# Performance work log

Measured on AMD Instinct MI355X. Metric: run time of the kernel, lower is better.

The kernel has to match this reference:

```python
import jax, jax.numpy as jnp
import numpy as np

B, L = 8, 512
D_MODEL, N_HEADS, N_LAYERS = 768, 12, 12
D_HEAD = D_MODEL // N_HEADS
D_FF = 4 * D_MODEL
NUM_LABELS = 1000
PATCH_DIM = 16 * 16 * 3
EPS = 1e-6


def setup_inputs() -> dict:
    key = jax.random.key(0)
    ks = jax.random.split(key, 24)
    d = D_MODEL

    def w(k, shape, fan_in):
        return (jax.random.normal(k, shape, jnp.float32) / np.sqrt(fan_in)).astype(jnp.float32)

    return {
        'patch': jax.random.normal(ks[0], (B, L, PATCH_DIM), jnp.float32),
        'box': jax.random.uniform(ks[1], (B, L, 4), jnp.float32),
        'patch_W': w(ks[2], (PATCH_DIM, d), PATCH_DIM),
        'patch_b': jnp.zeros((d,), jnp.float32),
        'box_W': w(ks[3], (d, d), d),
        'box_b': jnp.zeros((d,), jnp.float32),
        'Wq': w(ks[4], (N_LAYERS, d, d), d),
        'Wk': w(ks[5], (N_LAYERS, d, d), d),
        'Wv': w(ks[6], (N_LAYERS, d, d), d),
        'Wo': w(ks[7], (N_LAYERS, d, d), d),
        'attn_norm_w': jnp.ones((N_LAYERS, d), jnp.float32),
        'gate_W': w(ks[8], (N_LAYERS, d, D_FF), d),
        'hidden_W': w(ks[9], (N_LAYERS, d, D_FF), d),
        'ffn_out_W': w(ks[10], (N_LAYERS, D_FF, d), D_FF),
        'ffn_norm_w': jnp.ones((N_LAYERS, d), jnp.float32),
        'reward_norm_w': jnp.ones((d,), jnp.float32),
        'reward_W': w(ks[11], (d, 2), d),
        'reward_b': jnp.zeros((2,), jnp.float32),
        'label_norm_w': jnp.ones((d,), jnp.float32),
        'label_W': w(ks[12], (d, NUM_LABELS), d),
        'label_b': jnp.zeros((NUM_LABELS,), jnp.float32),
        'box_norm_w': jnp.ones((d,), jnp.float32),
        'boxh_W': w(ks[13], (d, 4), d),
        'boxh_b': jnp.zeros((4,), jnp.float32),
    }


def _rmsnorm(x, wgt):
    return x * jax.lax.rsqrt(jnp.mean(x * x, axis=-1, keepdims=True) + EPS) * wgt


def _rope(x, cos, sin):
    # x: [b, n, l, dh]; consecutive pairs form complex numbers (view_as_complex)
    xr, xi = x[..., 0::2], x[..., 1::2]
    out_r = xr * cos - xi * sin
    out_i = xr * sin + xi * cos
    return jnp.stack((out_r, out_i), axis=-1).reshape(x.shape)


def _forward(patch, box, patch_W, patch_b, box_W, box_b, Wq, Wk, Wv, Wo,
             attn_norm_w, gate_W, hidden_W, ffn_out_W, ffn_norm_w,
             reward_norm_w, reward_W, reward_b, label_norm_w, label_W, label_b,
             box_norm_w, boxh_W, boxh_b):
    b, l, _ = patch.shape
    d = D_MODEL
    # StackedSinusoidalEmbedding(d_model, 4): d_stack = d/4, theta over d_stack/2 freqs
    d_stack = d // 4
    theta_box = 1.0 / (10000.0 ** (2.0 * jnp.arange(d_stack // 2, dtype=jnp.float32) / d_stack))
    ang = box[..., None] * theta_box  # [b, l, 4, d_stack/2]
    box_sin = jnp.stack((jnp.cos(ang), jnp.sin(ang)), axis=-1).reshape(b, l, d)

    x = (patch @ patch_W + patch_b) + (box_sin @ box_W + box_b)

    # RoPE tables and causal mask (constants)
    theta = 1.0 / (10000.0 ** (2.0 * jnp.arange(D_HEAD // 2, dtype=jnp.float32) / D_HEAD))
    pos_ang = jnp.arange(l, dtype=jnp.float32)[:, None] * theta  # [l, dh/2]
    cos, sin = jnp.cos(pos_ang), jnp.sin(pos_ang)
    mask = jnp.triu(jnp.full((l, l), -jnp.inf, dtype=jnp.float32), 1)
    scale = jnp.float32(np.sqrt(D_HEAD))

    def block(h, p):
        wq, wk, wv, wo, anw, gw, hw, ow, fnw = p
        hn = _rmsnorm(h, anw)
        q = (hn @ wq).reshape(b, l, N_HEADS, D_HEAD).transpose(0, 2, 1, 3)
        k = (hn @ wk).reshape(b, l, N_HEADS, D_HEAD).transpose(0, 2, 1, 3)
        v = (hn @ wv).reshape(b, l, N_HEADS, D_HEAD).transpose(0, 2, 1, 3)
        scores = jnp.einsum('bnld,bnmd->bnlm', _rope(q, cos, sin), _rope(k, cos, sin)) / scale
        attn = jax.nn.softmax(scores + mask, axis=-1)
        o = jnp.einsum('bnlm,bnmd->bnld', attn, v).transpose(0, 2, 1, 3).reshape(b, l, d)
        h = h + o @ wo
        hn = _rmsnorm(h, fnw)
        h = h + (jax.nn.silu(hn @ gw) * (hn @ hw)) @ ow
        return h, None

    x, _ = jax.lax.scan(block, x, (Wq, Wk, Wv, Wo, attn_norm_w, gate_W, hidden_W, ffn_out_W, ffn_norm_w))

    reward = _rmsnorm(x, reward_norm_w) @ reward_W + reward_b
    label = _rmsnorm(x, label_norm_w) @ label_W + label_b
    box_out = _rmsnorm(x, box_norm_w) @ boxh_W + boxh_b
    return reward, label, box_out


def reference(patch, box, patch_W, patch_b, box_W, box_b, Wq, Wk, Wv, Wo,
              attn_norm_w, gate_W, hidden_W, ffn_out_W, ffn_norm_w,
              reward_norm_w, reward_W, reward_b, label_norm_w, label_W, label_b,
              box_norm_w, boxh_W, boxh_b):
    return _forward(patch, box, patch_W, patch_b, box_W, box_b, Wq, Wk, Wv, Wo,
                    attn_norm_w, gate_W, hidden_W, ffn_out_W, ffn_norm_w,
                    reward_norm_w, reward_W, reward_b, label_norm_w, label_W, label_b,
                    box_norm_w, boxh_W, boxh_b)
```

## Files before the change

### kernel.cpp

```cpp
#include <hip/hip_runtime.h>
#include <math.h>
#include <type_traits>

#define B_   8
#define L_   512
#define MTOK 4096
#define D_   768
#define NH_  12
#define DH_  64
#define DFF_ 3072
#define NL_  12

typedef unsigned short u16;
typedef __attribute__((ext_vector_type(4))) float f32x4;
typedef __attribute__((ext_vector_type(8))) short i16x8;
typedef __attribute__((ext_vector_type(8))) __bf16 b16x8;

template <typename A, typename = void>
struct PickFrag { using type = i16x8; };
template <typename A>
struct PickFrag<A, std::void_t<decltype(__builtin_amdgcn_mfma_f32_16x16x32_bf16(
    std::declval<A>(), std::declval<A>(), std::declval<f32x4>(), 0, 0, 0))>> {
  using type = A;
};
using frag_t = typename PickFrag<b16x8>::type;

#if __has_builtin(__builtin_amdgcn_global_load_lds)
#define HAS_GLDS 1
#else
#define HAS_GLDS 0
#endif

__device__ inline u16 f2bf(float f) {
    unsigned u = __float_as_uint(f);
    unsigned r = u + 0x7fffu + ((u >> 16) & 1u);
    return (u16)(r >> 16);
}
__device__ inline float bf2f(u16 b) { return __uint_as_float(((unsigned)b) << 16); }

__device__ inline void bar_raw() {
    asm volatile("" ::: "memory");
    __builtin_amdgcn_s_barrier();
    asm volatile("" ::: "memory");
}

__device__ inline int swz8(int row, int c8) { return c8 ^ ((row & 7) << 3); }

__device__ inline void glds16(const u16* g, u16* l) {
#if HAS_GLDS
    __builtin_amdgcn_global_load_lds(
        (const __attribute__((address_space(1))) void*)g,
        (__attribute__((address_space(3))) void*)l, 16, 0, 0);
#else
    *reinterpret_cast<uint4*>(l) = *reinterpret_cast<const uint4*>(g);
#endif
}

__global__ void k_box_sin(u16* __restrict__ emb, const float* __restrict__ box) {
    int idx = blockIdx.x * blockDim.x + threadIdx.x;
    if (idx >= MTOK * D_) return;
    int t = idx / D_, d = idx % D_;
    int c = d / 192, r = d % 192, j = r >> 1;
    float theta = __expf(-(float)j * (9.210340371976184f / 96.0f));
    float ang = box[t * 4 + c] * theta;
    emb[(size_t)t * 1536 + 768 + d] = f2bf((r & 1) ? sinf(ang) : cosf(ang));
}

__global__ void k_cast(u16* __restrict__ emb, const float* __restrict__ in, int n4) {
    int i = blockIdx.x * blockDim.x + threadIdx.x;
    if (i >= n4) return;
    int t = i / 192, c4 = (i % 192) * 4;
    float4 v = *reinterpret_cast<const float4*>(in + (size_t)t * 768 + c4);
    unsigned lo = (unsigned)f2bf(v.x) | ((unsigned)f2bf(v.y) << 16);
    unsigned hi = (unsigned)f2bf(v.z) | ((unsigned)f2bf(v.w) << 16);
    *reinterpret_cast<uint2*>(emb + (size_t)t * 1536 + c4) = make_uint2(lo, hi);
}

__global__ void k_addb(float* __restrict__ dst, const float* __restrict__ a,
                       const float* __restrict__ b) {
    int i = blockIdx.x * blockDim.x + threadIdx.x;
    if (i < D_) dst[i] = a[i] + b[i];
}

__global__ __launch_bounds__(256) void k_convT(u16* __restrict__ dst,
                                               const float* __restrict__ src,
                                               int K, int N, int ld, int rs,
                                               int ro, int co) {
    __shared__ float t[32][33];
    int bn = blockIdx.x * 32;
    int bk = blockIdx.y * 32;
    int tx = threadIdx.x % 32, ty = threadIdx.x / 32;
    #pragma unroll
    for (int i = 0; i < 4; ++i) {
        int k = bk + ty + i * 8;
        int n = bn + tx;
        t[ty + i * 8][tx] = (n < N) ? src[(size_t)k * N + n] : 0.0f;
    }
    __syncthreads();
    #pragma unroll
    for (int i = 0; i < 4; ++i) {
        int n = bn + ty + i * 8;
        int k = bk + tx;
        dst[(size_t)(n * rs + ro) * ld + co + k] = f2bf(t[tx][ty + i * 8]);
    }
}


__global__ __launch_bounds__(256) void k_convT128(u16* __restrict__ dst,
                                                  const float* __restrict__ src,
                                                  int K, int N) {
    __shared__ float ts[32][131];
    const float* s = src + (size_t)blockIdx.z * K * N;
    u16* d = dst + (size_t)blockIdx.z * K * N;
    int bn = blockIdx.x * 32, bk = blockIdx.y * 128;
    int t = threadIdx.x, rn = t & 31, kr = t >> 5;
    #pragma unroll
    for (int p = 0; p < 16; ++p) {
        int k = p * 8 + kr;
        ts[rn][k] = s[(size_t)(bk + k) * N + bn + rn];
    }
    __syncthreads();
    int n = t >> 3, c = (t & 7) * 8;
    u16 ta[8], tb[8];
    #pragma unroll
    for (int j = 0; j < 8; ++j) ta[j] = f2bf(ts[n][c + j]);
    #pragma unroll
    for (int j = 0; j < 8; ++j) tb[j] = f2bf(ts[n][64 + c + j]);
    u16* dp = &d[(size_t)(bn + n) * K + bk];
    *reinterpret_cast<uint4*>(dp + c)      = *reinterpret_cast<uint4*>(ta);
    *reinterpret_cast<uint4*>(dp + 64 + c) = *reinterpret_cast<uint4*>(tb);
}

__global__ __launch_bounds__(256) void k_convT128_qkv(u16* __restrict__ dst,
                                                      const float* __restrict__ s0,
                                                      const float* __restrict__ s1,
                                                      const float* __restrict__ s2) {
    __shared__ float ts[32][131];
    int ly = blockIdx.z / 3, which = blockIdx.z % 3;
    const float* s = (which == 0 ? s0 : (which == 1 ? s1 : s2)) + (size_t)ly * 768 * 768;
    u16* d = dst + ((size_t)ly * 3 + which) * 768 * 768;
    int bn = blockIdx.x * 32, bk = blockIdx.y * 128;
    int t = threadIdx.x, rn = t & 31, kr = t >> 5;
    #pragma unroll
    for (int p = 0; p < 16; ++p) {
        int k = p * 8 + kr;
        ts[rn][k] = s[(size_t)(bk + k) * 768 + bn + rn];
    }
    __syncthreads();
    int n = t >> 3, c = (t & 7) * 8;
    u16 ta[8], tb[8];
    #pragma unroll
    for (int j = 0; j < 8; ++j) ta[j] = f2bf(ts[n][c + j]);
    #pragma unroll
    for (int j = 0; j < 8; ++j) tb[j] = f2bf(ts[n][64 + c + j]);
    u16* dp = &d[(size_t)(bn + n) * 768 + bk];
    *reinterpret_cast<uint4*>(dp + c)      = *reinterpret_cast<uint4*>(ta);
    *reinterpret_cast<uint4*>(dp + 64 + c) = *reinterpret_cast<uint4*>(tb);
}

__global__ __launch_bounds__(256) void k_convT128_gh(u16* __restrict__ dst,
                                                     const float* __restrict__ g,
                                                     const float* __restrict__ h) {
    __shared__ float ts[32][131];
    int ly = blockIdx.z >> 1, which = blockIdx.z & 1;
    const float* s = (which ? h : g) + (size_t)ly * 768 * 3072;
    u16* d = dst + (size_t)ly * 6144 * 768;
    int bn = blockIdx.x * 32, bk = blockIdx.y * 128;
    int t = threadIdx.x, rn = t & 31, kr = t >> 5;
    #pragma unroll
    for (int p = 0; p < 16; ++p) {
        int k = p * 8 + kr;
        ts[rn][k] = s[(size_t)(bk + k) * 3072 + bn + rn];
    }
    __syncthreads();
    int n = t >> 3, c = (t & 7) * 8;
    int ng = bn + n;
    int row = ((ng >> 4) << 5) + (ng & 15) + which * 16;
    u16 ta[8], tb[8];
    #pragma unroll
    for (int j = 0; j < 8; ++j) ta[j] = f2bf(ts[n][c + j]);
    #pragma unroll
    for (int j = 0; j < 8; ++j) tb[j] = f2bf(ts[n][64 + c + j]);
    u16* dp = &d[(size_t)row * 768 + bk];
    *reinterpret_cast<uint4*>(dp + c)      = *reinterpret_cast<uint4*>(ta);
    *reinterpret_cast<uint4*>(dp + 64 + c) = *reinterpret_cast<uint4*>(tb);
}

template <int S>
__global__ __launch_bounds__(192) void k_fused_rr(float* __restrict__ h,
                                                  const float* __restrict__ part,
                                                  u16* __restrict__ hn,
                                                  const float* __restrict__ w) {
    int t = blockIdx.x;
    int i4 = threadIdx.x;
    size_t b4 = (size_t)t * 192 + i4;
    float4 v = reinterpret_cast<const float4*>(h)[b4];
    #pragma unroll
    for (int s = 0; s < S; ++s) {
        float4 p = reinterpret_cast<const float4*>(part + (size_t)s * MTOK * D_)[b4];
        v.x += p.x; v.y += p.y; v.z += p.z; v.w += p.w;
    }
    if (S > 0) reinterpret_cast<float4*>(h)[b4] = v;
    float ss = v.x * v.x + v.y * v.y + v.z * v.z + v.w * v.w;
    for (int off = 32; off > 0; off >>= 1) ss += __shfl_down(ss, off);
    __shared__ float red[3];
    int wid = threadIdx.x >> 6, lane = threadIdx.x & 63;
    if (lane == 0) red[wid] = ss;
    __syncthreads();
    float inv = rsqrtf((red[0] + red[1] + red[2]) / (float)D_ + 1e-6f);
    float4 wv = reinterpret_cast<const float4*>(w)[i4];
    unsigned lo = (unsigned)f2bf(v.x * inv * wv.x) | ((unsigned)f2bf(v.y * inv * wv.y) << 16);
    unsigned hi = (unsigned)f2bf(v.z * inv * wv.z) | ((unsigned)f2bf(v.w * inv * wv.w) << 16);
    *reinterpret_cast<uint2*>(hn + (size_t)t * D_ + i4 * 4) = make_uint2(lo, hi);
}

__global__ void k_rope_tab(float* __restrict__ tab) {
    int idx = blockIdx.x * blockDim.x + threadIdx.x;
    if (idx >= L_ * 32) return;
    int l = idx >> 5, j = idx & 31;
    float theta = __expf(-(float)j * (9.210340371976184f / 32.0f));
    float s, c;
    sincosf((float)l * theta, &s, &c);
    tab[idx * 2] = c;
    tab[idx * 2 + 1] = s;
}

__global__ __launch_bounds__(512) void k_gemm512_gh(u16* __restrict__ Cp,
                                                    const u16* __restrict__ A,
                                                    const u16* __restrict__ BT,
                                                    int K, int ldC) {
    __shared__ u16 smem[32768];
    int tid = threadIdx.x;
    int wid = tid >> 6, lane = tid & 63;

    int nx = gridDim.x, ny = gridDim.y;
    int bid = blockIdx.y * nx + blockIdx.x;
    int nwg = nx * ny;
    int cpx = nwg >> 3;
    int swzb = (bid & 7) * cpx + (bid >> 3);
    int by = swzb / nx, bx = swzb % nx;
    int row0 = by * 256, col0 = bx * 256;
    int wr = wid >> 2, wcn = wid & 3;

    int c0 = tid, c1 = tid + 512;
    int r0 = c0 >> 2, r1 = c1 >> 2;
    int gsrc = (((tid & 3) ^ ((tid >> 3) & 3)) << 3);
    const u16* gA0 = A  + (size_t)(row0 + r0) * K + gsrc;
    const u16* gA1 = A  + (size_t)(row0 + r1) * K + gsrc;
    const u16* gB0 = BT + (size_t)(col0 + r0) * K + gsrc;
    const u16* gB1 = BT + (size_t)(col0 + r1) * K + gsrc;

    auto stage = [&](int buf, int kt) {
        u16* Asb = smem + buf * 8192;
        u16* Bsb = smem + 16384 + buf * 8192;
        glds16(gA0 + kt, &Asb[c0 * 8]);
        glds16(gA1 + kt, &Asb[c1 * 8]);
        glds16(gB0 + kt, &Bsb[c0 * 8]);
        glds16(gB1 + kt, &Bsb[c1 * 8]);
    };

    f32x4 acc[8][4] = {};
    int lr = lane & 15, lg = lane >> 4;
    int lk = (((lg ^ ((lr >> 1) & 3))) << 3);

    stage(0, 0);
    int cur = 0;
    for (int kt = 0; kt < K; kt += 32) {
        bool has_next = (kt + 32 < K);
        if (has_next) stage(cur ^ 1, kt + 32);
        if (has_next) asm volatile("s_waitcnt vmcnt(4) lgkmcnt(0)" ::: "memory");
        else          asm volatile("s_waitcnt vmcnt(0) lgkmcnt(0)" ::: "memory");
        __builtin_amdgcn_sched_barrier(0);
        bar_raw();
        const u16* Asb = smem + cur * 8192;
        const u16* Bsb = smem + 16384 + cur * 8192;
        frag_t af[8], bfr[4];
        #pragma unroll
        for (int m = 0; m < 8; ++m)
            af[m] = *reinterpret_cast<const frag_t*>(&Asb[(wr * 128 + m * 16 + lr) * 32 + lk]);
        #pragma unroll
        for (int n = 0; n < 4; ++n)
            bfr[n] = *reinterpret_cast<const frag_t*>(&Bsb[(wcn * 64 + n * 16 + lr) * 32 + lk]);
        #pragma unroll
        for (int m = 0; m < 8; ++m)
            #pragma unroll
            for (int n = 0; n < 4; ++n)
                acc[m][n] = __builtin_amdgcn_mfma_f32_16x16x32_bf16(af[m], bfr[n], acc[m][n], 0, 0, 0);
        bar_raw();
        cur ^= 1;
    }

    int lcol = lane & 15, rb = (lane >> 4) * 4;
    #pragma unroll
    for (int m = 0; m < 8; ++m) {
        #pragma unroll
        for (int np = 0; np < 2; ++np) {
            int ocol = (col0 >> 1) + wcn * 32 + np * 16 + lcol;
            #pragma unroll
            for (int e = 0; e < 4; ++e) {
                int row = row0 + wr * 128 + m * 16 + rb + e;
                float g = acc[m][2 * np][e], hv = acc[m][2 * np + 1][e];
                float s = g / (1.0f + __expf(-g));
                Cp[(size_t)row * ldC + ocol] = f2bf(s * hv);
            }
        }
    }
}

template <int MODE>
__global__ __launch_bounds__(256) void k_gemm_bf16(void* __restrict__ Cp,
                                                   const u16* __restrict__ A,
                                                   const u16* __restrict__ BT,
                                                   const float* __restrict__ bias,
                                                   int K, int Nout, int ldC) {
    __shared__ u16 smem[16384];
    int tid = threadIdx.x;
    int wid = tid >> 6, lane = tid & 63;

    int nx = gridDim.x, ny = gridDim.y, nz = gridDim.z;
    int bid = ((blockIdx.z * ny) + blockIdx.y) * nx + blockIdx.x;
    int nwg = nx * ny * nz;
    int cpx = nwg >> 3;
    int swz = (bid & 7) * cpx + (bid >> 3);
    int sk  = swz / (nx * ny);
    int rem = swz % (nx * ny);
    int by = rem / nx, bx = rem % nx;
    int row0 = by * 128, col0 = bx * 128;
    int wr = wid >> 1, wc = wid & 1;

    int Klen = K / nz;
    int kbeg = sk * Klen;

    int c0 = wid * 128 + lane;
    int c1 = c0 + 64;
    int r0 = c0 >> 2, kc0 = (c0 & 3) * 8;
    int r1 = c1 >> 2, kc1 = (c1 & 3) * 8;
    const u16* gA0 = A  + (size_t)(row0 + r0) * K + kbeg + kc0;
    const u16* gA1 = A  + (size_t)(row0 + r1) * K + kbeg + kc1;
    const u16* gB0 = BT + (size_t)(col0 + r0) * K + kbeg + kc0;
    const u16* gB1 = BT + (size_t)(col0 + r1) * K + kbeg + kc1;

    auto stage = [&](int buf, int kt) {
        u16* Asb = smem + buf * 4096;
        u16* Bsb = smem + 8192 + buf * 4096;
        glds16(gA0 + kt, &Asb[c0 * 8]);
        glds16(gA1 + kt, &Asb[c1 * 8]);
        glds16(gB0 + kt, &Bsb[c0 * 8]);
        glds16(gB1 + kt, &Bsb[c1 * 8]);
    };

    f32x4 acc[4][4] = {};
    int lrow = lane & 15, lk = (lane >> 4) * 8;

    stage(0, 0);
    int cur = 0;
    for (int kt = 0; kt < Klen; kt += 32) {
        bool has_next = (kt + 32 < Klen);
        if (has_next) stage(cur ^ 1, kt + 32);
        if (has_next) asm volatile("s_waitcnt vmcnt(4) lgkmcnt(0)" ::: "memory");
        else          asm volatile("s_waitcnt vmcnt(0) lgkmcnt(0)" ::: "memory");
        __builtin_amdgcn_sched_barrier(0);
        bar_raw();
        const u16* Asb = smem + cur * 4096;
        const u16* Bsb = smem + 8192 + cur * 4096;
        frag_t af[4], bfr[4];
        #pragma unroll
        for (int m = 0; m < 4; ++m)
            af[m] = *reinterpret_cast<const frag_t*>(&Asb[(wr * 64 + m * 16 + lrow) * 32 + lk]);
        #pragma unroll
        for (int n = 0; n < 4; ++n)
            bfr[n] = *reinterpret_cast<const frag_t*>(&Bsb[(wc * 64 + n * 16 + lrow) * 32 + lk]);
        #pragma unroll
        for (int m = 0; m < 4; ++m)
            #pragma unroll
            for (int n = 0; n < 4; ++n)
                acc[m][n] = __builtin_amdgcn_mfma_f32_16x16x32_bf16(af[m], bfr[n], acc[m][n], 0, 0, 0);
        bar_raw();
        cur ^= 1;
    }

    int lcol = lane & 15, rb = (lane >> 4) * 4;

    if (MODE == 6) {
        u16* qkvh = (u16*)Cp;
        const float* tab = bias;
        if (col0 >= 1536) {
            int head_base = (col0 - 1536) >> 6;
            int bb = row0 >> 9;
            int l0 = row0 & 511;
            #pragma unroll
            for (int pass = 0; pass < 2; ++pass) {
                if (wc == pass) {
                    #pragma unroll
                    for (int m = 0; m < 4; ++m) {
                        #pragma unroll
                        for (int n = 0; n < 4; ++n) {
                            int dl = n * 16 + lcol;
                            int rl = wr * 64 + m * 16 + rb;
                            u16 tmp[4];
                            #pragma unroll
                            for (int e = 0; e < 4; ++e) tmp[e] = f2bf(acc[m][n][e]);
                            *reinterpret_cast<uint2*>(&smem[dl * 136 + rl]) =
                                *reinterpret_cast<uint2*>(tmp);
                        }
                    }
                }
                __syncthreads();
                int head = head_base + pass;
                size_t vbase = (size_t)2 * MTOK * 768 +
                               ((size_t)(bb * NH_ + head) * 64) * 512;
                #pragma unroll
                for (int it = 0; it < 4; ++it) {
                    int dd = it * 16 + (tid >> 4);
                    int rr = (tid & 15) * 8;
                    uint4 v4 = *reinterpret_cast<const uint4*>(&smem[dd * 136 + rr]);
                    *reinterpret_cast<uint4*>(&qkvh[vbase + (size_t)dd * 512 + l0 + rr]) = v4;
                }
                __syncthreads();
            }
        } else {
            int sec = col0 / 768;
            float qscale = (sec == 0) ? 0.125f : 1.0f;
            #pragma unroll
            for (int m = 0; m < 4; ++m) {
                #pragma unroll
                for (int n = 0; n < 4; ++n) {
                    int col = col0 + wc * 64 + n * 16 + lcol;
                    int head = (col % 768) >> 6;
                    int d = col & 63;
                    #pragma unroll
                    for (int e = 0; e < 4; ++e) {
                        int row = row0 + wr * 64 + m * 16 + rb + e;
                        int bb = row >> 9, l = row & 511;
                        float v = acc[m][n][e];
                        float p = __shfl_xor(v, 1);
                        float2 cs = *reinterpret_cast<const float2*>(
                            tab + ((size_t)l * 32 + (d >> 1)) * 2);
                        float r = (d & 1) ? (p * cs.y + v * cs.x)
                                          : (v * cs.x - p * cs.y);
                        r *= qscale;
                        qkvh[(size_t)sec * MTOK * 768 +
                             ((size_t)(bb * NH_ + head) * 512 + l) * 64 + d] = f2bf(r);
                    }
                }
            }
        }
        return;
    }

    float* Cpart = (MODE == 4)
        ? ((float*)Cp + (size_t)sk * (size_t)(ny * 128) * ldC) : (float*)Cp;
    #pragma unroll
    for (int m = 0; m < 4; ++m) {
        #pragma unroll
        for (int n = 0; n < 4; ++n) {
            int col = col0 + wc * 64 + n * 16 + lcol;
            if (col >= Nout) continue;
            #pragma unroll
            for (int e = 0; e < 4; ++e) {
                int row = row0 + wr * 64 + m * 16 + rb + e;
                float v = acc[m][n][e];
                size_t off = (size_t)row * ldC + col;
                if (MODE == 0) {
                    if (bias) v += bias[col];
                    ((float*)Cp)[off] = v;
                } else if (MODE == 3) {
                    ((u16*)Cp)[off] = f2bf(v);
                } else if (MODE == 4) {
                    Cpart[off] = v;
                }
            }
        }
    }
}

__global__ __launch_bounds__(256) void k_attn3(u16* __restrict__ o,
                                               const u16* __restrict__ qh,
                                               const u16* __restrict__ kh,
                                               const u16* __restrict__ vT) {
    int bh = blockIdx.x, qb = blockIdx.y;
    int b = bh / NH_, hh = bh % NH_;
    int tid = threadIdx.x, wid = tid >> 6, lane = tid & 63;
    __shared__ u16 Qs[64][72], Ps[64][72];
    __shared__ u16 Ks[64 * 64], Vs[64 * 64];

    #pragma unroll
    for (int i = 0; i < 2; ++i) {
        int idx = tid + i * 256;
        int r = idx >> 3, c8 = (idx & 7) * 8;
        uint4 v4 = *reinterpret_cast<const uint4*>(
            qh + ((size_t)bh * L_ + qb * 64 + r) * 64 + c8);
        *reinterpret_cast<uint4*>(&Qs[r][c8]) = v4;
    }
    __syncthreads();

    int lr = lane & 15, lg = lane >> 4;
    frag_t aq[2];
    #pragma unroll
    for (int kd = 0; kd < 2; ++kd)
        aq[kd] = *reinterpret_cast<const frag_t*>(&Qs[wid * 16 + lr][kd * 32 + lg * 8]);

    int sr0 = tid >> 3, sc8 = (tid & 7) * 8;
    int sr1 = sr0 + 32;

    f32x4 accO[4] = {};
    float M[4], S[4];
    #pragma unroll
    for (int e = 0; e < 4; ++e) { M[e] = -INFINITY; S[e] = 0.f; }

    uint4 kreg0 = *reinterpret_cast<const uint4*>(kh + ((size_t)bh * L_ + sr0) * 64 + sc8);
    uint4 kreg1 = *reinterpret_cast<const uint4*>(kh + ((size_t)bh * L_ + sr1) * 64 + sc8);
    uint4 vreg0 = *reinterpret_cast<const uint4*>(vT + ((size_t)bh * 64 + sr0) * L_ + sc8);
    uint4 vreg1 = *reinterpret_cast<const uint4*>(vT + ((size_t)bh * 64 + sr1) * L_ + sc8);

    for (int kb = 0; kb <= qb; ++kb) {
        __syncthreads();
        *reinterpret_cast<uint4*>(&Ks[sr0 * 64 + swz8(sr0, sc8)]) = kreg0;
        *reinterpret_cast<uint4*>(&Ks[sr1 * 64 + swz8(sr1, sc8)]) = kreg1;
        *reinterpret_cast<uint4*>(&Vs[sr0 * 64 + swz8(sr0, sc8)]) = vreg0;
        *reinterpret_cast<uint4*>(&Vs[sr1 * 64 + swz8(sr1, sc8)]) = vreg1;
        __syncthreads();
        if (kb < qb) {
            int nb = (kb + 1) * 64;
            kreg0 = *reinterpret_cast<const uint4*>(kh + ((size_t)bh * L_ + nb + sr0) * 64 + sc8);
            kreg1 = *reinterpret_cast<const uint4*>(kh + ((size_t)bh * L_ + nb + sr1) * 64 + sc8);
            vreg0 = *reinterpret_cast<const uint4*>(vT + ((size_t)bh * 64 + sr0) * L_ + nb + sc8);
            vreg1 = *reinterpret_cast<const uint4*>(vT + ((size_t)bh * 64 + sr1) * L_ + nb + sc8);
        }

        f32x4 sv[4];
        __builtin_amdgcn_s_setprio(1);
        #pragma unroll
        for (int ct = 0; ct < 4; ++ct) {
            int krow = ct * 16 + lr;
            frag_t bk0 = *reinterpret_cast<const frag_t*>(&Ks[krow * 64 + swz8(krow, lg * 8)]);
            frag_t bk1 = *reinterpret_cast<const frag_t*>(&Ks[krow * 64 + swz8(krow, 32 + lg * 8)]);
            f32x4 z = {0.f, 0.f, 0.f, 0.f};
            z = __builtin_amdgcn_mfma_f32_16x16x32_bf16(aq[0], bk0, z, 0, 0, 0);
            sv[ct] = __builtin_amdgcn_mfma_f32_16x16x32_bf16(aq[1], bk1, z, 0, 0, 0);
        }
        __builtin_amdgcn_s_setprio(0);

        bool diag = (kb == qb);
        float esc[4];
        #pragma unroll
        for (int e = 0; e < 4; ++e) {
            int qg = qb * 64 + wid * 16 + lg * 4 + e;
            float mx = -1e30f;
            #pragma unroll
            for (int ct = 0; ct < 4; ++ct) {
                float s = sv[ct][e];
                if (diag && (kb * 64 + ct * 16 + lr > qg)) s = -1e30f;
                sv[ct][e] = s;
                mx = fmaxf(mx, s);
            }
            #pragma unroll
            for (int msk = 8; msk; msk >>= 1) mx = fmaxf(mx, __shfl_xor(mx, msk));
            float newM = fmaxf(M[e], mx);
            float ps = 0.f;
            #pragma unroll
            for (int ct = 0; ct < 4; ++ct) {
                float p = __expf(sv[ct][e] - newM);
                sv[ct][e] = p;
                ps += p;
            }
            #pragma unroll
            for (int msk = 8; msk; msk >>= 1) ps += __shfl_xor(ps, msk);
            esc[e] = __expf(M[e] - newM);
            S[e] = S[e] * esc[e] + ps;
            M[e] = newM;
        }
        #pragma unroll
        for (int dt = 0; dt < 4; ++dt)
            #pragma unroll
            for (int e = 0; e < 4; ++e) accO[dt][e] *= esc[e];

        #pragma unroll
        for (int ct = 0; ct < 4; ++ct)
            #pragma unroll
            for (int e = 0; e < 4; ++e)
                Ps[wid * 16 + lg * 4 + e][ct * 16 + lr] = f2bf(sv[ct][e]);

        frag_t pa0 = *reinterpret_cast<const frag_t*>(&Ps[wid * 16 + lr][lg * 8]);
        frag_t pa1 = *reinterpret_cast<const frag_t*>(&Ps[wid * 16 + lr][32 + lg * 8]);
        __builtin_amdgcn_s_setprio(1);
        #pragma unroll
        for (int dt = 0; dt < 4; ++dt) {
            int vrow = dt * 16 + lr;
            frag_t bv0 = *reinterpret_cast<const frag_t*>(&Vs[vrow * 64 + swz8(vrow, lg * 8)]);
            frag_t bv1 = *reinterpret_cast<const frag_t*>(&Vs[vrow * 64 + swz8(vrow, 32 + lg * 8)]);
            accO[dt] = __builtin_amdgcn_mfma_f32_16x16x32_bf16(pa0, bv0, accO[dt], 0, 0, 0);
            accO[dt] = __builtin_amdgcn_mfma_f32_16x16x32_bf16(pa1, bv1, accO[dt], 0, 0, 0);
        }
        __builtin_amdgcn_s_setprio(0);
    }

    #pragma unroll
    for (int dt = 0; dt < 4; ++dt) {
        #pragma unroll
        for (int e = 0; e < 4; ++e) {
            int row = b * L_ + qb * 64 + wid * 16 + lg * 4 + e;
            o[(size_t)row * D_ + hh * 64 + dt * 16 + lr] = f2bf(accO[dt][e] / S[e]);
        }
    }
}

__global__ __launch_bounds__(256) void k_heads3(float* __restrict__ out_reward,
                                                float* __restrict__ out_box,
                                                const float* __restrict__ h,
                                                const float* __restrict__ rnw,
                                                const float* __restrict__ rW,
                                                const float* __restrict__ rb,
                                                const float* __restrict__ bnw,
                                                const float* __restrict__ bW,
                                                const float* __restrict__ bb) {
    int t = blockIdx.x;
    size_t base = (size_t)t * D_;
    float x[3];
    float ss = 0.f;
    #pragma unroll
    for (int c = 0; c < 3; ++c) {
        int i = threadIdx.x + c * 256;
        x[c] = h[base + i];
        ss += x[c] * x[c];
    }
    for (int off = 32; off > 0; off >>= 1) ss += __shfl_down(ss, off);
    __shared__ float red[4];
    int wid = threadIdx.x >> 6, lane = threadIdx.x & 63;
    if (lane == 0) red[wid] = ss;
    __syncthreads();
    float inv = rsqrtf((red[0] + red[1] + red[2] + red[3]) / (float)D_ + 1e-6f);

    float a[6] = {};
    #pragma unroll
    for (int c = 0; c < 3; ++c) {
        int i = threadIdx.x + c * 256;
        float xr = x[c] * inv;
        float xw = xr * rnw[i];
        a[0] += xw * rW[i * 2];
        a[1] += xw * rW[i * 2 + 1];
        float xb = xr * bnw[i];
        #pragma unroll
        for (int j = 0; j < 4; ++j) a[2 + j] += xb * bW[i * 4 + j];
    }
    #pragma unroll
    for (int j = 0; j < 6; ++j)
        for (int off = 32; off > 0; off >>= 1) a[j] += __shfl_down(a[j], off);
    __shared__ float red2[4][6];
    if (lane == 0)
        #pragma unroll
        for (int j = 0; j < 6; ++j) red2[wid][j] = a[j];
    __syncthreads();
    if (threadIdx.x < 6) {
        float s = red2[0][threadIdx.x] + red2[1][threadIdx.x] +
                  red2[2][threadIdx.x] + red2[3][threadIdx.x];
        if (threadIdx.x < 2) out_reward[(size_t)t * 2 + threadIdx.x] = s + rb[threadIdx.x];
        else                 out_box[(size_t)t * 4 + threadIdx.x - 2] = s + bb[threadIdx.x - 2];
    }
}

extern "C" void kernel_launch(void* const* d_in, const int* in_sizes, int n_in,
                              void* d_out, int out_size, void* d_ws, size_t ws_size,
                              hipStream_t stream) {
    const float* patch        = (const float*)d_in[0];
    const float* box          = (const float*)d_in[1];
    const float* patch_W      = (const float*)d_in[2];
    const float* patch_b      = (const float*)d_in[3];
    const float* box_W        = (const float*)d_in[4];
    const float* box_b        = (const float*)d_in[5];
    const float* Wq           = (const float*)d_in[6];
    const float* Wk           = (const float*)d_in[7];
    const float* Wv           = (const float*)d_in[8];
    const float* Wo           = (const float*)d_in[9];
    const float* attn_norm_w  = (const float*)d_in[10];
    const float* gate_W       = (const float*)d_in[11];
    const float* hidden_W     = (const float*)d_in[12];
    const float* ffn_out_W    = (const float*)d_in[13];
    const float* ffn_norm_w   = (const float*)d_in[14];
    const float* reward_norm_w= (const float*)d_in[15];
    const float* reward_W     = (const float*)d_in[16];
    const float* reward_b     = (const float*)d_in[17];
    const float* label_norm_w = (const float*)d_in[18];
    const float* label_W      = (const float*)d_in[19];
    const float* label_b      = (const float*)d_in[20];
    const float* box_norm_w   = (const float*)d_in[21];
    const float* boxh_W       = (const float*)d_in[22];
    const float* boxh_b       = (const float*)d_in[23];

    char* w = (char*)d_ws;
    auto alloc = [&](size_t bytes) { char* p = w; w += (bytes + 255) & ~(size_t)255; return p; };

    u16*  wqkv_a = (u16*)alloc((size_t)NL_ * 2304 * 768 * 2);
    u16*  wo_a   = (u16*)alloc((size_t)NL_ * 768 * 768 * 2);
    u16*  wgh_a  = (u16*)alloc((size_t)NL_ * 6144 * 768 * 2);
    u16*  wfo_a  = (u16*)alloc((size_t)NL_ * 768 * 3072 * 2);
    u16*  wcat   = (u16*)alloc((size_t)768 * 1536 * 2);
    u16*  wlab   = (u16*)alloc((size_t)1024 * 768 * 2);
    float* bias_c= (float*)alloc((size_t)768 * 4);
    u16*  emb    = (u16*)alloc((size_t)MTOK * 1536 * 2);
    float* h     = (float*)alloc((size_t)MTOK * D_ * 4);
    u16*  hn_bf  = (u16*)alloc((size_t)MTOK * D_ * 2);
    u16*  qkvh   = (u16*)alloc((size_t)MTOK * 2304 * 2);
    float* tab   = (float*)alloc((size_t)L_ * 32 * 2 * 4);
    u16*  o_bf   = (u16*)alloc((size_t)MTOK * D_ * 2);
    u16*  ga_bf  = (u16*)alloc((size_t)MTOK * DFF_ * 2);
    float* part  = (float*)alloc((size_t)4 * MTOK * D_ * 4);

    u16* qh = qkvh;
    u16* kh = qkvh + (size_t)MTOK * 768;
    u16* vT = qkvh + (size_t)2 * MTOK * 768;

    dim3 blk(256);

    k_convT<<<dim3(24, 24), blk, 0, stream>>>(wcat, patch_W, 768, 768, 1536, 1, 0, 0);
    k_convT<<<dim3(24, 24), blk, 0, stream>>>(wcat, box_W,   768, 768, 1536, 1, 0, 768);
    k_convT<<<dim3(32, 24), blk, 0, stream>>>(wlab, label_W, 768, 1000, 768, 1, 0, 0);
    k_addb<<<3, blk, 0, stream>>>(bias_c, patch_b, box_b);
    k_rope_tab<<<(L_ * 32 + 255) / 256, blk, 0, stream>>>(tab);
    k_convT128_qkv<<<dim3(24, 6, 36), blk, 0, stream>>>(wqkv_a, Wq, Wk, Wv);
    k_convT128<<<dim3(24, 6, 12), blk, 0, stream>>>(wo_a, Wo, 768, 768);
    k_convT128_gh<<<dim3(96, 6, 24), blk, 0, stream>>>(wgh_a, gate_W, hidden_W);
    k_convT128<<<dim3(24, 24, 12), blk, 0, stream>>>(wfo_a, ffn_out_W, 3072, 768);
    k_cast<<<(MTOK * 768 / 4 + 255) / 256, blk, 0, stream>>>(emb, patch, MTOK * 768 / 4);
    k_box_sin<<<(MTOK * D_ + 255) / 256, blk, 0, stream>>>(emb, box);

    k_gemm_bf16<0><<<dim3(6, 32), blk, 0, stream>>>(h, emb, wcat, bias_c, 1536, 768, 768);
    k_fused_rr<0><<<MTOK, dim3(192), 0, stream>>>(h, nullptr, hn_bf, attn_norm_w);

    for (int ly = 0; ly < NL_; ++ly) {
        const u16* wqkv = wqkv_a + (size_t)ly * 2304 * 768;
        const u16* wo_l = wo_a   + (size_t)ly * 768 * 768;
        const u16* wgh  = wgh_a  + (size_t)ly * 6144 * 768;
        const u16* wfo  = wfo_a  + (size_t)ly * 768 * 3072;
        const float* fnw = ffn_norm_w + (size_t)ly * D_;
        const float* nxt = (ly + 1 < NL_) ? attn_norm_w + (size_t)(ly + 1) * D_
                                          : label_norm_w;

        k_gemm_bf16<6><<<dim3(18, 32), blk, 0, stream>>>(qkvh, hn_bf, wqkv, tab, 768, 2304, 2304);
        k_attn3<<<dim3(96, 8), blk, 0, stream>>>(o_bf, qh, kh, vT);
        k_gemm_bf16<4><<<dim3(6, 32, 2), blk, 0, stream>>>(part, o_bf, wo_l, nullptr, 768, 768, 768);
        k_fused_rr<2><<<MTOK, dim3(192), 0, stream>>>(h, part, hn_bf, fnw);

        k_gemm512_gh<<<dim3(24, 16), dim3(512), 0, stream>>>(ga_bf, hn_bf, wgh, 768, 3072);
        k_gemm_bf16<4><<<dim3(6, 32, 4), blk, 0, stream>>>(part, ga_bf, wfo, nullptr, 3072, 768, 768);
        k_fused_rr<4><<<MTOK, dim3(192), 0, stream>>>(h, part, hn_bf, nxt);
    }

    float* out_reward = (float*)d_out;
    float* out_label  = out_reward + (size_t)MTOK * 2;
    float* out_box    = out_label + (size_t)MTOK * 1000;

    k_gemm_bf16<0><<<dim3(8, 32), blk, 0, stream>>>(out_label, hn_bf, wlab, label_b, 768, 1000, 1000);
    k_heads3<<<MTOK, blk, 0, stream>>>(out_reward, out_box, h,
                                       reward_norm_w, reward_W, reward_b,
                                       box_norm_w, boxh_W, boxh_b);
}
```

Baseline: 2.306 ms.

## Use exp2 softmax with lazy rescale, fuse Wo residual add, halve FFN split-K

The attention kernel now works in the base-2 domain: log2(e) is folded into the Q scale, and the code skips the running-max rescale of the accumulator when no row max grows within a wave. The Wo projection adds directly into the residual stream through a new accumulate mode instead of writing split-K partials and reducing them in the norm kernel. The FFN-out GEMM split-K drops from 4 to 2. Together these cut exp work, rescale multiplies and partial-buffer traffic, at the cost of fewer blocks for the Wo GEMM and the FFN-out GEMM.

```diff
diff --git a/kernel.cpp b/kernel.cpp
--- a/kernel.cpp
+++ b/kernel.cpp
@@ -30,6 +30,8 @@
 #else
 #define HAS_GLDS 0
 #endif
+
+#define LOG2E 1.44269504088896340736f
 
 __device__ inline u16 f2bf(float f) {
     unsigned u = __float_as_uint(f);
@@ -420,7 +422,7 @@
             }
         } else {
             int sec = col0 / 768;
-            float qscale = (sec == 0) ? 0.125f : 1.0f;
+            float qscale = (sec == 0) ? 0.125f * LOG2E : 1.0f;
             #pragma unroll
             for (int m = 0; m < 4; ++m) {
                 #pragma unroll
@@ -464,6 +466,8 @@
                 if (MODE == 0) {
                     if (bias) v += bias[col];
                     ((float*)Cp)[off] = v;
+                } else if (MODE == 1) {
+                    ((float*)Cp)[off] += v;
                 } else if (MODE == 3) {
                     ((u16*)Cp)[off] = f2bf(v);
                 } else if (MODE == 4) {
@@ -542,7 +546,7 @@
         __builtin_amdgcn_s_setprio(0);
 
         bool diag = (kb == qb);
-        float esc[4];
+        float mxv[4];
         #pragma unroll
         for (int e = 0; e < 4; ++e) {
             int qg = qb * 64 + wid * 16 + lg * 4 + e;
@@ -556,24 +560,44 @@
             }
             #pragma unroll
             for (int msk = 8; msk; msk >>= 1) mx = fmaxf(mx, __shfl_xor(mx, msk));
-            float newM = fmaxf(M[e], mx);
-            float ps = 0.f;
-            #pragma unroll
-            for (int ct = 0; ct < 4; ++ct) {
-                float p = __expf(sv[ct][e] - newM);
-                sv[ct][e] = p;
-                ps += p;
+            mxv[e] = mx;
+        }
+        bool grow = (mxv[0] > M[0]) | (mxv[1] > M[1]) |
+                    (mxv[2] > M[2]) | (mxv[3] > M[3]);
+        if (__any(grow)) {
+            #pragma unroll
+            for (int e = 0; e < 4; ++e) {
+                float newM = fmaxf(M[e], mxv[e]);
+                float ps = 0.f;
+                #pragma unroll
+                for (int ct = 0; ct < 4; ++ct) {
+                    float p = exp2f(sv[ct][e] - newM);
+                    sv[ct][e] = p;
+                    ps += p;
+                }
+                #pragma unroll
+                for (int msk = 8; msk; msk >>= 1) ps += __shfl_xor(ps, msk);
+                float esc = exp2f(M[e] - newM);
+                S[e] = S[e] * esc + ps;
+                M[e] = newM;
+                #pragma unroll
+                for (int dt = 0; dt < 4; ++dt) accO[dt][e] *= esc;
             }
-            #pragma unroll
-            for (int msk = 8; msk; msk >>= 1) ps += __shfl_xor(ps, msk);
-            esc[e] = __expf(M[e] - newM);
-            S[e] = S[e] * esc[e] + ps;
-            M[e] = newM;
-        }
-        #pragma unroll
-        for (int dt = 0; dt < 4; ++dt)
-            #pragma unroll
-            for (int e = 0; e < 4; ++e) accO[dt][e] *= esc[e];
+        } else {
+            #pragma unroll
+            for (int e = 0; e < 4; ++e) {
+                float ps = 0.f;
+                #pragma unroll
+                for (int ct = 0; ct < 4; ++ct) {
+                    float p = exp2f(sv[ct][e] - M[e]);
+                    sv[ct][e] = p;
+                    ps += p;
+                }
+                #pragma unroll
+                for (int msk = 8; msk; msk >>= 1) ps += __shfl_xor(ps, msk);
+                S[e] += ps;
+            }
+        }
 
         #pragma unroll
         for (int ct = 0; ct < 4; ++ct)
@@ -738,12 +762,12 @@
 
         k_gemm_bf16<6><<<dim3(18, 32), blk, 0, stream>>>(qkvh, hn_bf, wqkv, tab, 768, 2304, 2304);
         k_attn3<<<dim3(96, 8), blk, 0, stream>>>(o_bf, qh, kh, vT);
-        k_gemm_bf16<4><<<dim3(6, 32, 2), blk, 0, stream>>>(part, o_bf, wo_l, nullptr, 768, 768, 768);
-        k_fused_rr<2><<<MTOK, dim3(192), 0, stream>>>(h, part, hn_bf, fnw);
+        k_gemm_bf16<1><<<dim3(6, 32), blk, 0, stream>>>(h, o_bf, wo_l, nullptr, 768, 768, 768);
+        k_fused_rr<0><<<MTOK, dim3(192), 0, stream>>>(h, nullptr, hn_bf, fnw);
 
         k_gemm512_gh<<<dim3(24, 16), dim3(512), 0, stream>>>(ga_bf, hn_bf, wgh, 768, 3072);
-        k_gemm_bf16<4><<<dim3(6, 32, 4), blk, 0, stream>>>(part, ga_bf, wfo, nullptr, 3072, 768, 768);
-        k_fused_rr<4><<<MTOK, dim3(192), 0, stream>>>(h, part, hn_bf, nxt);
+        k_gemm_bf16<4><<<dim3(6, 32, 2), blk, 0, stream>>>(part, ga_bf, wfo, nullptr, 3072, 768, 768);
+        k_fused_rr<2><<<MTOK, dim3(192), 0, stream>>>(h, part, hn_bf, nxt);
     }
 
     float* out_reward = (float*)d_out;
```

Result: slower. 2.455 ms (+6.5%).
